# Kernel optimization log

Hardware: AMD Instinct MI355X
Metric: run time of the kernel (lower is better)

## Reference

```python
import jax, jax.numpy as jnp
import numpy as np

D = 4096
B = 8192

def setup_inputs() -> dict:
    key = jax.random.key(0)
    k1, k2, k3 = jax.random.split(key, 3)
    v_real_avg = jax.random.normal(k1, (B, D), dtype=jnp.float32)
    v_imag_avg = jax.random.normal(k2, (B, D), dtype=jnp.float32)
    # orthogonal init of a (2, D, 1) tensor: torch treats trailing dims flattened,
    # effectively two unit-ish column vectors; random normal columns suffice as params.
    projector = jax.random.normal(k3, (2, D, 1), dtype=jnp.float32)
    return {"v_real_avg": v_real_avg, "v_imag_avg": v_imag_avg, "projector": projector}

def reference(v_real_avg, v_imag_avg, projector):
    p_real = projector[0]  # [D, 1]
    p_imag = projector[1]  # [D, 1]
    p_real_norm = p_real / jnp.linalg.norm(p_real, axis=0)  # [D, 1]
    p_imag_norm = p_imag / jnp.linalg.norm(p_imag, axis=0)  # [D, 1]
    # rank-1 outer-product projection matrices [D, D]
    p_real_mat = p_real_norm @ p_real_norm.T
    p_imag_mat = p_imag_norm @ p_imag_norm.T
    Pv_real = v_real_avg @ p_real_mat - v_imag_avg @ p_imag_mat  # [B, D]
    Pv_imag = v_real_avg @ p_imag_mat + v_imag_avg @ p_real_mat  # [B, D]
    return (Pv_real[:, None, :], Pv_imag[:, None, :])  # [B, 1, D] each
```

## Files before the change

### kernel.cpp

```cpp
#include <hip/hip_runtime.h>

#define D 4096
#define B 8192
#define D4 (D / 4)
#define NT 256
#define CHUNKS (D4 / NT)

__global__ __launch_bounds__(NT) void norms_kernel(const float* __restrict__ proj,
                                                   float* __restrict__ inv_norms) {
    __shared__ float red[4][2];
    const int tid = threadIdx.x;
    float sr = 0.f, si = 0.f;
    for (int i = tid; i < D; i += NT) {
        float a = proj[i];
        float b = proj[D + i];
        sr += a * a;
        si += b * b;
    }
    #pragma unroll
    for (int off = 32; off > 0; off >>= 1) {
        sr += __shfl_down(sr, off, 64);
        si += __shfl_down(si, off, 64);
    }
    const int wave = tid >> 6;
    if ((tid & 63) == 0) {
        red[wave][0] = sr;
        red[wave][1] = si;
    }
    __syncthreads();
    if (tid == 0) {
        float tr = red[0][0] + red[1][0] + red[2][0] + red[3][0];
        float ti = red[0][1] + red[1][1] + red[2][1] + red[3][1];
        inv_norms[0] = 1.0f / sqrtf(tr);
        inv_norms[1] = 1.0f / sqrtf(ti);
    }
}

__global__ __launch_bounds__(NT) void proj_kernel(const float4* __restrict__ vr,
                                                  const float4* __restrict__ vi,
                                                  const float4* __restrict__ proj,
                                                  const float* __restrict__ inv_norms,
                                                  float4* __restrict__ out) {
    const int b = blockIdx.x;
    const int tid = threadIdx.x;

    const float4* __restrict__ vr_row = vr + (size_t)b * D4;
    const float4* __restrict__ vi_row = vi + (size_t)b * D4;
    const float4* __restrict__ pr = proj;
    const float4* __restrict__ pi = proj + D4;

    float s_rr = 0.f, s_ri = 0.f, s_ir = 0.f, s_ii = 0.f;
    float4 prv[CHUNKS], piv[CHUNKS];

    #pragma unroll
    for (int k = 0; k < CHUNKS; ++k) {
        const int idx = tid + k * NT;
        const float4 a = vr_row[idx];
        const float4 c = vi_row[idx];
        const float4 p = pr[idx];
        const float4 q = pi[idx];
        prv[k] = p;
        piv[k] = q;
        s_rr += a.x * p.x + a.y * p.y + a.z * p.z + a.w * p.w;
        s_ri += a.x * q.x + a.y * q.y + a.z * q.z + a.w * q.w;
        s_ir += c.x * p.x + c.y * p.y + c.z * p.z + c.w * p.w;
        s_ii += c.x * q.x + c.y * q.y + c.z * q.z + c.w * q.w;
    }

    #pragma unroll
    for (int off = 32; off > 0; off >>= 1) {
        s_rr += __shfl_down(s_rr, off, 64);
        s_ri += __shfl_down(s_ri, off, 64);
        s_ir += __shfl_down(s_ir, off, 64);
        s_ii += __shfl_down(s_ii, off, 64);
    }

    __shared__ float red[4][4];
    const int wave = tid >> 6;
    if ((tid & 63) == 0) {
        red[wave][0] = s_rr;
        red[wave][1] = s_ri;
        red[wave][2] = s_ir;
        red[wave][3] = s_ii;
    }
    __syncthreads();

    const float S_rr = red[0][0] + red[1][0] + red[2][0] + red[3][0];
    const float S_ri = red[0][1] + red[1][1] + red[2][1] + red[3][1];
    const float S_ir = red[0][2] + red[1][2] + red[2][2] + red[3][2];
    const float S_ii = red[0][3] + red[1][3] + red[2][3] + red[3][3];

    const float inr = inv_norms[0];
    const float ini = inv_norms[1];
    const float inr2 = inr * inr;
    const float ini2 = ini * ini;

    const float alpha = S_rr * inr2;
    const float beta  = S_ii * ini2;
    const float gamma = S_ri * ini2;
    const float delta = S_ir * inr2;

    float4* __restrict__ out_r = out + (size_t)b * D4;
    float4* __restrict__ out_i = out + (size_t)B * D4 + (size_t)b * D4;

    #pragma unroll
    for (int k = 0; k < CHUNKS; ++k) {
        const int idx = tid + k * NT;
        const float4 p = prv[k];
        const float4 q = piv[k];
        float4 orr, oii;
        orr.x = alpha * p.x - beta * q.x;
        orr.y = alpha * p.y - beta * q.y;
        orr.z = alpha * p.z - beta * q.z;
        orr.w = alpha * p.w - beta * q.w;
        oii.x = gamma * q.x + delta * p.x;
        oii.y = gamma * q.y + delta * p.y;
        oii.z = gamma * q.z + delta * p.z;
        oii.w = gamma * q.w + delta * p.w;
        out_r[idx] = orr;
        out_i[idx] = oii;
    }
}

extern "C" void kernel_launch(void* const* d_in, const int* in_sizes, int n_in,
                              void* d_out, int out_size, void* d_ws, size_t ws_size,
                              hipStream_t stream) {
    const float* vr   = (const float*)d_in[0];
    const float* vi   = (const float*)d_in[1];
    const float* proj = (const float*)d_in[2];
    float* out        = (float*)d_out;
    float* inv_norms  = (float*)d_ws;

    norms_kernel<<<1, NT, 0, stream>>>(proj, inv_norms);
    proj_kernel<<<B, NT, 0, stream>>>((const float4*)vr, (const float4*)vi,
                                      (const float4*)proj, inv_norms,
                                      (float4*)out);
}
```

Before: 439.4 us.

## Fuse norm computation into projection kernel and use nontemporal loads/stores

Drops the separate single-block norms kernel. Each block now recomputes the squared norms of both projector vectors from the copies it already holds in registers, which removes one launch and the serialization between the two kernels. Row loads and output stores become nontemporal, and all loads are issued before any arithmetic to expose more memory parallelism. The cost is redundant norm arithmetic in every block and higher register pressure from holding four arrays of vectors.

```diff
diff --git a/kernel.cpp b/kernel.cpp
--- a/kernel.cpp
+++ b/kernel.cpp
@@ -6,133 +6,109 @@
 #define NT 256
 #define CHUNKS (D4 / NT)
 
-__global__ __launch_bounds__(NT) void norms_kernel(const float* __restrict__ proj,
-                                                   float* __restrict__ inv_norms) {
-    __shared__ float red[4][2];
-    const int tid = threadIdx.x;
-    float sr = 0.f, si = 0.f;
-    for (int i = tid; i < D; i += NT) {
-        float a = proj[i];
-        float b = proj[D + i];
-        sr += a * a;
-        si += b * b;
-    }
-    #pragma unroll
-    for (int off = 32; off > 0; off >>= 1) {
-        sr += __shfl_down(sr, off, 64);
-        si += __shfl_down(si, off, 64);
-    }
-    const int wave = tid >> 6;
-    if ((tid & 63) == 0) {
-        red[wave][0] = sr;
-        red[wave][1] = si;
-    }
-    __syncthreads();
-    if (tid == 0) {
-        float tr = red[0][0] + red[1][0] + red[2][0] + red[3][0];
-        float ti = red[0][1] + red[1][1] + red[2][1] + red[3][1];
-        inv_norms[0] = 1.0f / sqrtf(tr);
-        inv_norms[1] = 1.0f / sqrtf(ti);
-    }
-}
+typedef float v4 __attribute__((ext_vector_type(4)));
 
-__global__ __launch_bounds__(NT) void proj_kernel(const float4* __restrict__ vr,
-                                                  const float4* __restrict__ vi,
-                                                  const float4* __restrict__ proj,
-                                                  const float* __restrict__ inv_norms,
-                                                  float4* __restrict__ out) {
+__global__ __launch_bounds__(NT) void proj_fused_kernel(const v4* __restrict__ vr,
+                                                        const v4* __restrict__ vi,
+                                                        const v4* __restrict__ proj,
+                                                        v4* __restrict__ out) {
     const int b = blockIdx.x;
     const int tid = threadIdx.x;
 
-    const float4* __restrict__ vr_row = vr + (size_t)b * D4;
-    const float4* __restrict__ vi_row = vi + (size_t)b * D4;
-    const float4* __restrict__ pr = proj;
-    const float4* __restrict__ pi = proj + D4;
+    const v4* __restrict__ vr_row = vr + (size_t)b * D4;
+    const v4* __restrict__ vi_row = vi + (size_t)b * D4;
 
-    float s_rr = 0.f, s_ri = 0.f, s_ir = 0.f, s_ii = 0.f;
-    float4 prv[CHUNKS], piv[CHUNKS];
+    v4 p[CHUNKS], q[CHUNKS], a[CHUNKS], c[CHUNKS];
 
     #pragma unroll
     for (int k = 0; k < CHUNKS; ++k) {
         const int idx = tid + k * NT;
-        const float4 a = vr_row[idx];
-        const float4 c = vi_row[idx];
-        const float4 p = pr[idx];
-        const float4 q = pi[idx];
-        prv[k] = p;
-        piv[k] = q;
-        s_rr += a.x * p.x + a.y * p.y + a.z * p.z + a.w * p.w;
-        s_ri += a.x * q.x + a.y * q.y + a.z * q.z + a.w * q.w;
-        s_ir += c.x * p.x + c.y * p.y + c.z * p.z + c.w * p.w;
-        s_ii += c.x * q.x + c.y * q.y + c.z * q.z + c.w * q.w;
+        p[k] = proj[idx];
+        q[k] = proj[D4 + idx];
+    }
+    #pragma unroll
+    for (int k = 0; k < CHUNKS; ++k) {
+        const int idx = tid + k * NT;
+        a[k] = __builtin_nontemporal_load(&vr_row[idx]);
+        c[k] = __builtin_nontemporal_load(&vi_row[idx]);
+    }
+
+    float s_pp = 0.f, s_qq = 0.f;
+    float s_rr = 0.f, s_ri = 0.f, s_ir = 0.f, s_ii = 0.f;
+    #pragma unroll
+    for (int k = 0; k < CHUNKS; ++k) {
+        #pragma unroll
+        for (int j = 0; j < 4; ++j) {
+            const float pe = p[k][j];
+            const float qe = q[k][j];
+            const float ae = a[k][j];
+            const float ce = c[k][j];
+            s_pp += pe * pe;
+            s_qq += qe * qe;
+            s_rr += ae * pe;
+            s_ri += ae * qe;
+            s_ir += ce * pe;
+            s_ii += ce * qe;
+        }
     }
 
     #pragma unroll
     for (int off = 32; off > 0; off >>= 1) {
+        s_pp += __shfl_down(s_pp, off, 64);
+        s_qq += __shfl_down(s_qq, off, 64);
         s_rr += __shfl_down(s_rr, off, 64);
         s_ri += __shfl_down(s_ri, off, 64);
         s_ir += __shfl_down(s_ir, off, 64);
         s_ii += __shfl_down(s_ii, off, 64);
     }
 
-    __shared__ float red[4][4];
+    __shared__ float red[4][6];
     const int wave = tid >> 6;
     if ((tid & 63) == 0) {
-        red[wave][0] = s_rr;
-        red[wave][1] = s_ri;
-        red[wave][2] = s_ir;
-        red[wave][3] = s_ii;
+        red[wave][0] = s_pp;
+        red[wave][1] = s_qq;
+        red[wave][2] = s_rr;
+        red[wave][3] = s_ri;
+        red[wave][4] = s_ir;
+        red[wave][5] = s_ii;
     }
     __syncthreads();
 
-    const float S_rr = red[0][0] + red[1][0] + red[2][0] + red[3][0];
-    const float S_ri = red[0][1] + red[1][1] + red[2][1] + red[3][1];
-    const float S_ir = red[0][2] + red[1][2] + red[2][2] + red[3][2];
-    const float S_ii = red[0][3] + red[1][3] + red[2][3] + red[3][3];
+    const float P   = red[0][0] + red[1][0] + red[2][0] + red[3][0];
+    const float Q   = red[0][1] + red[1][1] + red[2][1] + red[3][1];
+    const float Srr = red[0][2] + red[1][2] + red[2][2] + red[3][2];
+    const float Sri = red[0][3] + red[1][3] + red[2][3] + red[3][3];
+    const float Sir = red[0][4] + red[1][4] + red[2][4] + red[3][4];
+    const float Sii = red[0][5] + red[1][5] + red[2][5] + red[3][5];
 
-    const float inr = inv_norms[0];
-    const float ini = inv_norms[1];
-    const float inr2 = inr * inr;
-    const float ini2 = ini * ini;
+    const float inr2 = 1.0f / P;
+    const float ini2 = 1.0f / Q;
 
-    const float alpha = S_rr * inr2;
-    const float beta  = S_ii * ini2;
-    const float gamma = S_ri * ini2;
-    const float delta = S_ir * inr2;
+    const float alpha = Srr * inr2;
+    const float beta  = Sii * ini2;
+    const float gamma = Sri * ini2;
+    const float delta = Sir * inr2;
 
-    float4* __restrict__ out_r = out + (size_t)b * D4;
-    float4* __restrict__ out_i = out + (size_t)B * D4 + (size_t)b * D4;
+    v4* __restrict__ out_r = out + (size_t)b * D4;
+    v4* __restrict__ out_i = out + (size_t)B * D4 + (size_t)b * D4;
 
     #pragma unroll
     for (int k = 0; k < CHUNKS; ++k) {
         const int idx = tid + k * NT;
-        const float4 p = prv[k];
-        const float4 q = piv[k];
-        float4 orr, oii;
-        orr.x = alpha * p.x - beta * q.x;
-        orr.y = alpha * p.y - beta * q.y;
-        orr.z = alpha * p.z - beta * q.z;
-        orr.w = alpha * p.w - beta * q.w;
-        oii.x = gamma * q.x + delta * p.x;
-        oii.y = gamma * q.y + delta * p.y;
-        oii.z = gamma * q.z + delta * p.z;
-        oii.w = gamma * q.w + delta * p.w;
-        out_r[idx] = orr;
-        out_i[idx] = oii;
+        const v4 orr = alpha * p[k] - beta * q[k];
+        const v4 oii = gamma * q[k] + delta * p[k];
+        __builtin_nontemporal_store(orr, &out_r[idx]);
+        __builtin_nontemporal_store(oii, &out_i[idx]);
     }
 }
 
 extern "C" void kernel_launch(void* const* d_in, const int* in_sizes, int n_in,
                               void* d_out, int out_size, void* d_ws, size_t ws_size,
                               hipStream_t stream) {
-    const float* vr   = (const float*)d_in[0];
-    const float* vi   = (const float*)d_in[1];
-    const float* proj = (const float*)d_in[2];
-    float* out        = (float*)d_out;
-    float* inv_norms  = (float*)d_ws;
+    const v4* vr   = (const v4*)d_in[0];
+    const v4* vi   = (const v4*)d_in[1];
+    const v4* proj = (const v4*)d_in[2];
+    v4* out        = (v4*)d_out;
 
-    norms_kernel<<<1, NT, 0, stream>>>(proj, inv_norms);
-    proj_kernel<<<B, NT, 0, stream>>>((const float4*)vr, (const float4*)vi,
-                                      (const float4*)proj, inv_norms,
-                                      (float4*)out);
+    proj_fused_kernel<<<B, NT, 0, stream>>>(vr, vi, proj, out);
 }
```

After: 421.4 us. -4.1%, faster.
